# Kernel tuning notes

Hardware: AMD Instinct MI355X
Metric: run time of the kernel (lower is better)

Reference implementation:

```python
import jax, jax.numpy as jnp
import numpy as np

P = 16          # patch size (patch_height == patch_width)
DIM = 768       # feature dim
K = 9           # number of anchor boxes (arange(0, 9) in source)
# anchor_boxes = [(h_ratio, w_ratio) for h in (2,4,8) for w in (2,4,8)]
BOX_H = jnp.array([2., 2., 2., 4., 4., 4., 8., 8., 8.], dtype=jnp.float32)
BOX_W = jnp.array([2., 4., 8., 2., 4., 8., 2., 4., 8.], dtype=jnp.float32)


def setup_inputs() -> dict:
    key = jax.random.key(0)
    k0, k1, k2, k3 = jax.random.split(key, 4)
    b, c, h, w = 32, 3, 512, 512
    img = jax.random.normal(k0, (b, c, h, w), dtype=jnp.float32)
    # patch-embed stand-in for feature_extraction_ViT: (c*P*P) -> DIM
    w_patch = jax.random.normal(k1, (c * P * P, DIM), dtype=jnp.float32) * 0.02
    w_reg = jax.random.normal(k2, (DIM, 4 * K), dtype=jnp.float32) * 0.02
    b_reg = jnp.zeros((4 * K,), dtype=jnp.float32)
    w_obj = jax.random.normal(k3, (DIM, K), dtype=jnp.float32) * 0.02
    b_obj = jnp.zeros((K,), dtype=jnp.float32)
    return {"img": img, "w_patch": w_patch, "w_reg": w_reg, "b_reg": b_reg,
            "w_obj": w_obj, "b_obj": b_obj}


def reference(img, w_patch, w_reg, b_reg, w_obj, b_obj):
    b, c, h, w = img.shape
    fh, fw = h // P, w // P
    # --- feature_extraction_ViT (patch embedding) -> feature map [b, fh, fw, DIM]
    patches = img.reshape(b, c, fh, P, fw, P).transpose(0, 2, 4, 1, 3, 5)
    patches = patches.reshape(b, fh, fw, c * P * P)
    feat = patches @ w_patch                                  # [b, fh, fw, DIM]
    # --- RPN: regs [b, fh, fw, K, 4], objectness [b, fh, fw, K, 1]
    regs = (feat @ w_reg + b_reg).reshape(b, fh, fw, K, 4)    # separate_anchor_boxes, s=4
    is_object = jax.nn.sigmoid(feat @ w_obj + b_obj)[..., None]
    # --- anchor-box coordinate decoding (memory-bound broadcast pipeline)
    wgrid = jnp.arange(0, w, P, dtype=jnp.float32)            # step = patch_width
    hgrid = jnp.arange(0, h, P, dtype=jnp.float32)            # step = patch_height
    width_coords = wgrid[None, None, :, None, None] + regs[..., 0:1]
    height_coords = hgrid[None, :, None, None, None] + regs[..., 1:2]
    width_abs = width_coords + BOX_W[None, None, None, :, None] * regs[..., 2:3]
    height_abs = height_coords + BOX_H[None, None, None, :, None] * regs[..., 3:4]
    batch_idx = jnp.broadcast_to(
        jnp.arange(b, dtype=jnp.float32)[:, None, None, None, None], (b, fh, fw, K, 1))
    k_idx = jnp.broadcast_to(
        jnp.arange(K, dtype=jnp.float32)[None, None, None, :, None], (b, fh, fw, K, 1))
    merged = jnp.concatenate(
        [width_coords, height_coords, width_abs, height_abs, batch_idx, is_object, k_idx],
        axis=-1)                                              # [b, fh, fw, K, 7]
    tensor_reshaped = merged.reshape(-1, 7)                   # (b h w k) x
    return tensor_reshaped
```

## Files before the change

kernel.cpp:

```cpp
#include <hip/hip_runtime.h>

typedef __attribute__((ext_vector_type(8))) short bf16x8;
typedef __attribute__((ext_vector_type(4))) float f32x4;

__device__ __forceinline__ unsigned short f2bf(float f) {
    unsigned int u = __float_as_uint(f);
    u = (u + 0x7FFFu + ((u >> 16) & 1u)) >> 16;
    return (unsigned short)u;
}

__global__ __launch_bounds__(256) void wcomb_partial(
        const float* __restrict__ wp, const float* __restrict__ wreg,
        const float* __restrict__ wobj, float* __restrict__ part) {
    __shared__ float Al[64][132];
    __shared__ float Bl[48][132];
    const int t  = threadIdx.x;
    const int d0 = blockIdx.x * 128;
    const int k0 = blockIdx.y * 64;

    #pragma unroll
    for (int i = 0; i < 8; ++i) {
        int e = i * 256 + t;
        int row = e >> 5, dq = e & 31;
        *(f32x4*)&Al[row][dq * 4] =
            *(const f32x4*)&wp[(size_t)(k0 + row) * 768 + d0 + dq * 4];
    }
    #pragma unroll
    for (int i = 0; i < 24; ++i) {
        int e = i * 256 + t;
        int d = e / 48, n = e - d * 48;
        float v = 0.f;
        if (n < 36)      v = wreg[(size_t)(d0 + d) * 36 + n];
        else if (n < 45) v = wobj[(size_t)(d0 + d) * 9 + (n - 36)];
        Bl[n][d] = v;
    }
    __syncthreads();

    const int r0 = (t & 15) * 4;
    const int n0 = (t >> 4) * 3;
    float acc[4][3] = {};
    for (int ds = 0; ds < 32; ++ds) {
        f32x4 a[4], bv[3];
        #pragma unroll
        for (int i = 0; i < 4; ++i) a[i] = *(const f32x4*)&Al[r0 + i][ds * 4];
        #pragma unroll
        for (int j = 0; j < 3; ++j) bv[j] = *(const f32x4*)&Bl[n0 + j][ds * 4];
        #pragma unroll
        for (int i = 0; i < 4; ++i)
            #pragma unroll
            for (int j = 0; j < 3; ++j)
                acc[i][j] += a[i].x * bv[j].x + a[i].y * bv[j].y
                           + a[i].z * bv[j].z + a[i].w * bv[j].w;
    }
    #pragma unroll
    for (int i = 0; i < 4; ++i)
        #pragma unroll
        for (int j = 0; j < 3; ++j)
            part[((size_t)blockIdx.x * 768 + k0 + r0 + i) * 48 + n0 + j] = acc[i][j];
}

__global__ __launch_bounds__(256) void wcomb_reduce(
        const float* __restrict__ part, unsigned short* __restrict__ wct) {
    const int k = blockIdx.x * 256 + threadIdx.x;
    const int n = blockIdx.y;
    float s = 0.f;
    if (n < 45) {
        #pragma unroll
        for (int dc = 0; dc < 6; ++dc) s += part[((size_t)dc * 768 + k) * 48 + n];
    }
    wct[(size_t)n * 768 + k] = f2bf(s);
}

__global__ __launch_bounds__(256) void detector_main(
        const float* __restrict__ img, const unsigned short* __restrict__ wct,
        const float* __restrict__ breg, const float* __restrict__ bobj,
        float* __restrict__ out) {
    __shared__ unsigned short A[64][72];
    __shared__ float Co[64][49];

    const int t    = threadIdx.x;
    const int lane = t & 63;
    const int wid  = t >> 6;
    const int cl   = lane & 15;
    const int q    = lane >> 4;
    const int b    = blockIdx.x >> 4;
    const int fi0  = (blockIdx.x & 15) * 2;
    const float* img_b = img + (size_t)b * 3 * 512 * 512;

    f32x4 acc[3];
    #pragma unroll
    for (int nt = 0; nt < 3; ++nt) acc[nt] = (f32x4){0.f, 0.f, 0.f, 0.f};

    for (int cc = 0; cc < 12; ++cc) {
        const int c  = cc >> 2;
        const int p0 = (cc & 3) * 4;
        #pragma unroll
        for (int it = 0; it < 2; ++it) {
            int s      = it * 256 + t;
            int row_id = s >> 6, seg = s & 63;
            int fl = row_id >> 2, p = row_id & 3;
            int fj = seg >> 1,    g = seg & 1;
            const float* src = img_b
                + ((size_t)c * 512 + (fi0 + fl) * 16 + p0 + p) * 512 + fj * 16 + g * 8;
            f32x4 v0 = *(const f32x4*)src;
            f32x4 v1 = *(const f32x4*)(src + 4);
            bf16x8 w;
            w[0] = (short)f2bf(v0.x); w[1] = (short)f2bf(v0.y);
            w[2] = (short)f2bf(v0.z); w[3] = (short)f2bf(v0.w);
            w[4] = (short)f2bf(v1.x); w[5] = (short)f2bf(v1.y);
            w[6] = (short)f2bf(v1.z); w[7] = (short)f2bf(v1.w);
            *(bf16x8*)&A[fl * 32 + fj][p * 16 + g * 8] = w;
        }
        __syncthreads();
        const int kb = cc * 64 + q * 8;
        #pragma unroll
        for (int ks = 0; ks < 2; ++ks) {
            bf16x8 af = *(const bf16x8*)&A[wid * 16 + cl][ks * 32 + q * 8];
            #pragma unroll
            for (int nt = 0; nt < 3; ++nt) {
                bf16x8 bfr = *(const bf16x8*)&wct[(size_t)(nt * 16 + cl) * 768 + kb + ks * 32];
                acc[nt] = __builtin_amdgcn_mfma_f32_16x16x32_bf16(af, bfr, acc[nt], 0, 0, 0);
            }
        }
        __syncthreads();
    }

    #pragma unroll
    for (int nt = 0; nt < 3; ++nt)
        #pragma unroll
        for (int r = 0; r < 4; ++r)
            Co[wid * 16 + q * 4 + r][nt * 16 + cl] = acc[nt][r];
    __syncthreads();

    for (int rr = t; rr < 576; rr += 256) {
        int cell = rr / 9, k = rr - cell * 9;
        int fl = cell >> 5, fj = cell & 31;
        int fi = fi0 + fl;
        float v0 = Co[cell][4 * k + 0] + breg[4 * k + 0];
        float v1 = Co[cell][4 * k + 1] + breg[4 * k + 1];
        float v2 = Co[cell][4 * k + 2] + breg[4 * k + 2];
        float v3 = Co[cell][4 * k + 3] + breg[4 * k + 3];
        float lg = Co[cell][36 + k] + bobj[k];
        float obj = 1.f / (1.f + __expf(-lg));
        float wc = (float)(fj * 16) + v0;
        float hc = (float)(fi * 16) + v1;
        float wa = wc + (float)(2 << (k % 3)) * v2;
        float ha = hc + (float)(2 << (k / 3)) * v3;
        float* o = out + (size_t)(((b * 32 + fi) * 32 + fj) * 9 + k) * 7;
        o[0] = wc; o[1] = hc; o[2] = wa; o[3] = ha;
        o[4] = (float)b; o[5] = obj; o[6] = (float)k;
    }
}

extern "C" void kernel_launch(void* const* d_in, const int* in_sizes, int n_in,
                              void* d_out, int out_size, void* d_ws, size_t ws_size,
                              hipStream_t stream) {
    const float* img  = (const float*)d_in[0];
    const float* wp   = (const float*)d_in[1];
    const float* wreg = (const float*)d_in[2];
    const float* breg = (const float*)d_in[3];
    const float* wobj = (const float*)d_in[4];
    const float* bobj = (const float*)d_in[5];
    float* out = (float*)d_out;

    float* part = (float*)d_ws;
    unsigned short* wct = (unsigned short*)((char*)d_ws + 6 * 768 * 48 * 4);

    wcomb_partial<<<dim3(6, 12), 256, 0, stream>>>(wp, wreg, wobj, part);
    wcomb_reduce<<<dim3(3, 48), 256, 0, stream>>>(part, wct);
    detector_main<<<512, 256, 0, stream>>>(img, wct, breg, bobj, out);
}
```

Baseline: 187.5 us.

## Load image fragments directly into MFMA registers with software prefetch, dropping LDS staging

The main detector kernel no longer stages converted image patches through shared memory with two block barriers per K-chunk. Each wave now owns 16 cells, reads its A fragment straight from global memory into registers, converts to bf16 in-register, and double-buffers both A and weight fragments one step ahead. The epilogue is made per-wave as well. This removes LDS traffic and barrier stalls but gives up coalescing: each lane reads 32-byte segments strided across rows, which may increase memory transactions.

```diff
diff --git a/kernel.cpp b/kernel.cpp
--- a/kernel.cpp
+++ b/kernel.cpp
@@ -75,7 +75,6 @@
         const float* __restrict__ img, const unsigned short* __restrict__ wct,
         const float* __restrict__ breg, const float* __restrict__ bobj,
         float* __restrict__ out) {
-    __shared__ unsigned short A[64][72];
     __shared__ float Co[64][49];
 
     const int t    = threadIdx.x;
@@ -83,64 +82,63 @@
     const int wid  = t >> 6;
     const int cl   = lane & 15;
     const int q    = lane >> 4;
-    const int b    = blockIdx.x >> 4;
-    const int fi0  = (blockIdx.x & 15) * 2;
-    const float* img_b = img + (size_t)b * 3 * 512 * 512;
+    const int wg   = blockIdx.x * 4 + wid;
+    const int fj0  = (wg & 1) * 16;
+    const int fi   = (wg >> 1) & 31;
+    const int b    = wg >> 6;
 
-    f32x4 acc[3];
-    #pragma unroll
-    for (int nt = 0; nt < 3; ++nt) acc[nt] = (f32x4){0.f, 0.f, 0.f, 0.f};
+    const float* ap = img + (size_t)b * 786432
+        + (size_t)(fi * 16 + (q >> 1)) * 512 + (fj0 + cl) * 16 + (q & 1) * 8;
+    const unsigned short* bp = wct + cl * 768 + q * 8;
 
-    for (int cc = 0; cc < 12; ++cc) {
-        const int c  = cc >> 2;
-        const int p0 = (cc & 3) * 4;
-        #pragma unroll
-        for (int it = 0; it < 2; ++it) {
-            int s      = it * 256 + t;
-            int row_id = s >> 6, seg = s & 63;
-            int fl = row_id >> 2, p = row_id & 3;
-            int fj = seg >> 1,    g = seg & 1;
-            const float* src = img_b
-                + ((size_t)c * 512 + (fi0 + fl) * 16 + p0 + p) * 512 + fj * 16 + g * 8;
-            f32x4 v0 = *(const f32x4*)src;
-            f32x4 v1 = *(const f32x4*)(src + 4);
-            bf16x8 w;
-            w[0] = (short)f2bf(v0.x); w[1] = (short)f2bf(v0.y);
-            w[2] = (short)f2bf(v0.z); w[3] = (short)f2bf(v0.w);
-            w[4] = (short)f2bf(v1.x); w[5] = (short)f2bf(v1.y);
-            w[6] = (short)f2bf(v1.z); w[7] = (short)f2bf(v1.w);
-            *(bf16x8*)&A[fl * 32 + fj][p * 16 + g * 8] = w;
-        }
-        __syncthreads();
-        const int kb = cc * 64 + q * 8;
-        #pragma unroll
-        for (int ks = 0; ks < 2; ++ks) {
-            bf16x8 af = *(const bf16x8*)&A[wid * 16 + cl][ks * 32 + q * 8];
-            #pragma unroll
-            for (int nt = 0; nt < 3; ++nt) {
-                bf16x8 bfr = *(const bf16x8*)&wct[(size_t)(nt * 16 + cl) * 768 + kb + ks * 32];
-                acc[nt] = __builtin_amdgcn_mfma_f32_16x16x32_bf16(af, bfr, acc[nt], 0, 0, 0);
-            }
-        }
-        __syncthreads();
+    f32x4 acc0 = {0.f,0.f,0.f,0.f}, acc1 = acc0, acc2 = acc0;
+
+    f32x4 ca0 = *(const f32x4*)ap;
+    f32x4 ca1 = *(const f32x4*)(ap + 4);
+    bf16x8 cb0 = *(const bf16x8*)(bp);
+    bf16x8 cb1 = *(const bf16x8*)(bp + 12288);
+    bf16x8 cb2 = *(const bf16x8*)(bp + 24576);
+
+    #pragma unroll 4
+    for (int kk = 0; kk < 24; ++kk) {
+        const int astep = ((kk & 7) == 7) ? 254976 : 1024;
+        const float* nap = (kk == 23) ? ap : ap + astep;
+        const unsigned short* nbp = (kk == 23) ? bp : bp + 32;
+        f32x4 na0 = *(const f32x4*)nap;
+        f32x4 na1 = *(const f32x4*)(nap + 4);
+        bf16x8 nb0 = *(const bf16x8*)(nbp);
+        bf16x8 nb1 = *(const bf16x8*)(nbp + 12288);
+        bf16x8 nb2 = *(const bf16x8*)(nbp + 24576);
+
+        bf16x8 af;
+        af[0] = (short)f2bf(ca0.x); af[1] = (short)f2bf(ca0.y);
+        af[2] = (short)f2bf(ca0.z); af[3] = (short)f2bf(ca0.w);
+        af[4] = (short)f2bf(ca1.x); af[5] = (short)f2bf(ca1.y);
+        af[6] = (short)f2bf(ca1.z); af[7] = (short)f2bf(ca1.w);
+        acc0 = __builtin_amdgcn_mfma_f32_16x16x32_bf16(af, cb0, acc0, 0, 0, 0);
+        acc1 = __builtin_amdgcn_mfma_f32_16x16x32_bf16(af, cb1, acc1, 0, 0, 0);
+        acc2 = __builtin_amdgcn_mfma_f32_16x16x32_bf16(af, cb2, acc2, 0, 0, 0);
+
+        ap = nap; bp = nbp;
+        ca0 = na0; ca1 = na1; cb0 = nb0; cb1 = nb1; cb2 = nb2;
     }
 
     #pragma unroll
-    for (int nt = 0; nt < 3; ++nt)
-        #pragma unroll
-        for (int r = 0; r < 4; ++r)
-            Co[wid * 16 + q * 4 + r][nt * 16 + cl] = acc[nt][r];
+    for (int r = 0; r < 4; ++r) {
+        Co[wid * 16 + q * 4 + r][ 0 + cl] = acc0[r];
+        Co[wid * 16 + q * 4 + r][16 + cl] = acc1[r];
+        Co[wid * 16 + q * 4 + r][32 + cl] = acc2[r];
+    }
     __syncthreads();
 
-    for (int rr = t; rr < 576; rr += 256) {
+    for (int rr = lane; rr < 144; rr += 64) {
         int cell = rr / 9, k = rr - cell * 9;
-        int fl = cell >> 5, fj = cell & 31;
-        int fi = fi0 + fl;
-        float v0 = Co[cell][4 * k + 0] + breg[4 * k + 0];
-        float v1 = Co[cell][4 * k + 1] + breg[4 * k + 1];
-        float v2 = Co[cell][4 * k + 2] + breg[4 * k + 2];
-        float v3 = Co[cell][4 * k + 3] + breg[4 * k + 3];
-        float lg = Co[cell][36 + k] + bobj[k];
+        int fj = fj0 + cell;
+        float v0 = Co[wid * 16 + cell][4 * k + 0] + breg[4 * k + 0];
+        float v1 = Co[wid * 16 + cell][4 * k + 1] + breg[4 * k + 1];
+        float v2 = Co[wid * 16 + cell][4 * k + 2] + breg[4 * k + 2];
+        float v3 = Co[wid * 16 + cell][4 * k + 3] + breg[4 * k + 3];
+        float lg = Co[wid * 16 + cell][36 + k] + bobj[k];
         float obj = 1.f / (1.f + __expf(-lg));
         float wc = (float)(fj * 16) + v0;
         float hc = (float)(fi * 16) + v1;
```

Measured after the change: 189.2 us. No clear change (+0.9%).
